# Kernel tuning notes

Hardware: AMD Instinct MI355X
Metric: run time of the kernel (lower is better)

The kernel has to match this reference:

```python
import jax, jax.numpy as jnp
import numpy as np

N, E, D, L = 50000, 600000, 128, 3
EPS = 1e-5


def _layer_norm(x, g, b):
    m = jnp.mean(x, axis=-1, keepdims=True)
    v = jnp.mean((x - m) ** 2, axis=-1, keepdims=True)
    return (x - m) * jax.lax.rsqrt(v + EPS) * g + b


def setup_inputs() -> dict:
    key = jax.random.key(0)
    ks = jax.random.split(key, 20)
    s = 1.0 / np.sqrt(D)
    inp = {
        "node": jax.random.normal(ks[0], (N, D), jnp.float32),
        "edge_attr": jax.random.uniform(ks[1], (E,), jnp.float32),
        # stacked per-layer parameters [L, ...]
        "W_rel": jax.random.uniform(ks[2], (L, D, D), jnp.float32, -s, s),
        "b_rel": jax.random.uniform(ks[3], (L, D), jnp.float32, -s, s),
        "W_root": jax.random.uniform(ks[4], (L, D, D), jnp.float32, -s, s),
        "ln1_g": jnp.ones((L, D), jnp.float32),
        "ln1_b": jnp.zeros((L, D), jnp.float32),
        "ln2_g": jnp.ones((L, D), jnp.float32),
        "ln2_b": jnp.zeros((L, D), jnp.float32),
        "W1": jax.random.uniform(ks[5], (L, D, D), jnp.float32, -s, s),
        "b1": jax.random.uniform(ks[6], (L, D), jnp.float32, -s, s),
        "W2": jax.random.uniform(ks[7], (L, D, D), jnp.float32, -s, s),
        "b2": jax.random.uniform(ks[8], (L, D), jnp.float32, -s, s),
        "jk_W": jax.random.uniform(ks[9], (L * D, D), jnp.float32, -1.0 / np.sqrt(L * D), 1.0 / np.sqrt(L * D)),
        "jk_b": jax.random.uniform(ks[10], (D,), jnp.float32, -1.0 / np.sqrt(L * D), 1.0 / np.sqrt(L * D)),
        "edge_index": jax.random.randint(ks[11], (2, E), 0, N, jnp.int64),
        "batch_ptr": jnp.sort(jax.random.randint(ks[12], (51,), 0, N, jnp.int64)),
    }
    return inp


def reference(node, edge_attr, W_rel, b_rel, W_root, ln1_g, ln1_b, ln2_g, ln2_b,
              W1, b1, W2, b2, jk_W, jk_b, edge_index, batch_ptr):
    src, dst = edge_index[0], edge_index[1]
    deg = jax.ops.segment_sum(jnp.ones((E,), node.dtype), dst, num_segments=N)
    inv_deg = 1.0 / jnp.maximum(deg, 1.0)  # nodes with no in-edges -> 0 aggregate
    outs = []
    for l in range(L):
        msg = node[src] * edge_attr[:, None]                       # [E, D] gather
        agg = jax.ops.segment_sum(msg, dst, num_segments=N)        # scatter-sum
        mean = agg * inv_deg[:, None]                              # mean aggregation
        # GraphConv: lin_rel(aggr) + lin_root(x); skip_connection=False
        node = mean @ W_rel[l] + b_rel[l] + node @ W_root[l]
        node = jax.nn.relu(_layer_norm(node @ W1[l] + b1[l], ln1_g[l], ln1_b[l]))
        node = jax.nn.relu(_layer_norm(node @ W2[l] + b2[l], ln2_g[l], ln2_b[l]))
        outs.append(node)
    jk = jnp.concatenate(outs, axis=-1)                            # [N, L*D]
    return jk @ jk_W + jk_b
```

## Files before the change

kernel.cpp:

```cpp
#include <hip/hip_runtime.h>

#define NN 50000
#define EE 600000
#define DD 128
#define CAP 64
#define BINS 196
#define NP (BINS * 256)
#define BINCAP 3584
#define BCSTRIDE 16
#define LDS_STRIDE 136
#define P1_EDGES 2048
#define P1_BLOCKS ((EE + P1_EDGES - 1) / P1_EDGES)

typedef __attribute__((ext_vector_type(8))) short bf16x8;
typedef __attribute__((ext_vector_type(4))) float f32x4;

__device__ __forceinline__ unsigned short f2bf(float f) {
    union { float f; unsigned u; } v; v.f = f;
    unsigned r = v.u + 0x7FFF + ((v.u >> 16) & 1);
    return (unsigned short)(r >> 16);
}
__device__ __forceinline__ float bflo(unsigned x) { return __uint_as_float(x << 16); }
__device__ __forceinline__ float bfhi(unsigned x) { return __uint_as_float(x & 0xffff0000u); }

__global__ __launch_bounds__(256) void fill_p1(
    const int* __restrict__ src, const int* __restrict__ dst, const float* __restrict__ ea,
    int* __restrict__ binCnt, unsigned long long* __restrict__ recs) {
    __shared__ int hist[BINS];
    __shared__ int lstart[BINS];
    __shared__ int gbase[BINS];
    __shared__ int scan[256];
    __shared__ unsigned long long srt[P1_EDGES];
    const int t = threadIdx.x;
    for (int i = t; i < BINS; i += 256) hist[i] = 0;
    __syncthreads();

    unsigned long long rec[8];
    int bin[8], rnk[8];
    bool val[8];
#pragma unroll
    for (int g = 0; g < 2; ++g) {
        int e0 = blockIdx.x * P1_EDGES + g * 1024 + t * 4;
        int4 dv, sv; float4 ev;
        if (e0 + 3 < EE) {
            dv = *(const int4*)&dst[e0];
            sv = *(const int4*)&src[e0];
            ev = *(const float4*)&ea[e0];
        } else {
            int* dp = (int*)&dv; int* sp = (int*)&sv; float* ep = (float*)&ev;
#pragma unroll
            for (int k = 0; k < 4; ++k) {
                int e = e0 + k;
                dp[k] = (e < EE) ? dst[e] : 0;
                sp[k] = (e < EE) ? src[e] : 0;
                ep[k] = (e < EE) ? ea[e] : 0.f;
            }
        }
#pragma unroll
        for (int k = 0; k < 4; ++k) {
            int i = g * 4 + k;
            int e = e0 + k;
            val[i] = (e < EE);
            int d = ((const int*)&dv)[k];
            unsigned w16 = (unsigned)__float2int_rn(((const float*)&ev)[k] * 65535.0f);
            if (w16 > 65535u) w16 = 65535u;
            rec[i] = ((unsigned long long)(unsigned)d << 32) |
                     (((unsigned)((const int*)&sv)[k]) << 16) | w16;
            bin[i] = d >> 8;
            rnk[i] = val[i] ? atomicAdd(&hist[bin[i]], 1) : 0;
        }
    }
    __syncthreads();
    scan[t] = (t < BINS) ? hist[t] : 0;
    __syncthreads();
#pragma unroll
    for (int off = 1; off < 256; off <<= 1) {
        int v = (t >= off) ? scan[t - off] : 0;
        __syncthreads();
        scan[t] += v;
        __syncthreads();
    }
    if (t < BINS) {
        lstart[t] = scan[t] - hist[t];
        gbase[t] = hist[t] ? atomicAdd(&binCnt[t * BCSTRIDE], hist[t]) : 0;
    }
    __syncthreads();
#pragma unroll
    for (int i = 0; i < 8; ++i)
        if (val[i]) srt[lstart[bin[i]] + rnk[i]] = rec[i];
    __syncthreads();
    const int total = scan[255];
    for (int j = t; j < total; j += 256) {
        unsigned long long r = srt[j];
        int b = (int)(r >> 40);
        int o = gbase[b] + (j - lstart[b]);
        if (o < BINCAP) recs[(size_t)b * BINCAP + o] = r;
    }
}

__global__ __launch_bounds__(256) void fill_p2(
    const int* __restrict__ binCnt, const unsigned long long* __restrict__ recs,
    int* __restrict__ cnt, unsigned* __restrict__ slots) {
    __shared__ int cl[128];
    __shared__ unsigned sl[128 * CAP];
    const int b = blockIdx.x >> 1, half = blockIdx.x & 1, t = threadIdx.x;
    if (t < 128) cl[t] = 0;
    __syncthreads();
    int n = binCnt[b * BCSTRIDE];
    if (n > BINCAP) n = BINCAP;
    const unsigned long long* rp = recs + (size_t)b * BINCAP;
    for (int j = t; j < n; j += 256) {
        unsigned long long r = rp[j];
        int dl = (int)(r >> 32) & 255;
        if ((dl >> 7) == half) {
            int p = atomicAdd(&cl[dl & 127], 1);
            if (p < CAP) sl[(dl & 127) * CAP + p] = (unsigned)r;
        }
    }
    __syncthreads();
    const int node0 = (b << 8) + (half << 7);
    if (t < 128) cnt[node0 + t] = cl[t];
    const uint4* s4 = (const uint4*)sl;
    uint4* g4 = (uint4*)(slots + (size_t)node0 * CAP);
    for (int i = t; i < 2048; i += 256) g4[i] = s4[i];
}

#define CONV_BLKS 6250
__global__ void prep_kernel(const float* __restrict__ nodef, unsigned short* __restrict__ node_bf,
                            const float* __restrict__ W_rel, const float* __restrict__ W_root,
                            const float* __restrict__ W1, const float* __restrict__ W2,
                            const float* __restrict__ jkW,
                            const float* __restrict__ b_rel, const float* __restrict__ b1,
                            float* __restrict__ bc, unsigned short* __restrict__ packed) {
    int b = blockIdx.x;
    if (b < 96) {
        int tg = b * 256 + threadIdx.x;
        int chunk = tg >> 11, r = tg & 2047;
        int lane = r & 63, tile = r >> 6;
        int kt = tile >> 3, nt = tile & 7;
        int quad = lane >> 4, n = lane & 15;
        int k0 = kt * 32 + quad * 8;
        int col = nt * 16 + n;
        union { unsigned short u[8]; uint4 v; } tmp;
        if (chunk < 6) {
            int l = (chunk < 3) ? chunk : chunk - 3;
            const float* A = ((chunk < 3) ? W_rel : W_root) + (size_t)l * 16384;
            const float* B = W1 + (size_t)l * 16384;
            float acc[8] = {0.f, 0.f, 0.f, 0.f, 0.f, 0.f, 0.f, 0.f};
            for (int k = 0; k < 128; ++k) {
                float bv = B[k * 128 + col];
#pragma unroll
                for (int j = 0; j < 8; ++j) acc[j] = fmaf(A[(k0 + j) * 128 + k], bv, acc[j]);
            }
#pragma unroll
            for (int j = 0; j < 8; ++j) tmp.u[j] = f2bf(acc[j]);
        } else {
            const float* s = (chunk < 9) ? (W2 + (size_t)(chunk - 6) * 16384)
                                         : (jkW + (size_t)(chunk - 9) * 16384);
#pragma unroll
            for (int j = 0; j < 8; ++j) tmp.u[j] = f2bf(s[(size_t)(k0 + j) * DD + col]);
        }
        *(uint4*)&packed[(size_t)tg * 8] = tmp.v;
    } else if (b == 96) {
        for (int o = threadIdx.x; o < 384; o += 256) {
            int l = o >> 7, j = o & 127;
            float s = 0.f;
            for (int k = 0; k < 128; ++k)
                s = fmaf(b_rel[l * 128 + k], W1[(size_t)l * 16384 + k * 128 + j], s);
            bc[o] = s + b1[o];
        }
    } else {
        int i = (b - 97) * 256 + threadIdx.x;
        float4 v = *(const float4*)&nodef[(size_t)i * 4];
        ushort4 o;
        o.x = f2bf(v.x); o.y = f2bf(v.y); o.z = f2bf(v.z); o.w = f2bf(v.w);
        *(ushort4*)&node_bf[(size_t)i * 4] = o;
    }
}

__global__ __launch_bounds__(256) void gather_mean_kernel(
    const unsigned short* __restrict__ feat,
    const unsigned* __restrict__ slots,
    const int* __restrict__ cnt,
    unsigned short* __restrict__ mean) {
    const int node = (int)((blockIdx.x * 256 + threadIdx.x) >> 6);
    if (node >= NN) return;
    const int lane = threadIdx.x & 63;
    const int g  = lane >> 4;
    const int h8 = (lane & 15) * 8;
    int c = cnt[node];
    if (c > CAP) c = CAP;
    const unsigned* sp = slots + (size_t)node * CAP;

    float acc[8] = {0.f, 0.f, 0.f, 0.f, 0.f, 0.f, 0.f, 0.f};
    const float wscale = 1.0f / 65535.0f;

    for (int j0 = 0; j0 < c; j0 += 16) {
        uint4 sv = *(const uint4*)&sp[j0 + g * 4];
        unsigned se[4] = {sv.x, sv.y, sv.z, sv.w};
#pragma unroll
        for (int t = 0; t < 4; ++t) {
            int idx = j0 + g * 4 + t;
            bool ok = idx < c;
            unsigned e = se[t];
            int   srcn = ok ? (int)(e >> 16) : 0;
            float w    = ok ? (float)(e & 0xffffu) * wscale : 0.0f;
            uint4 v = *(const uint4*)&feat[(size_t)srcn * DD + h8];
            acc[0] = fmaf(bflo(v.x), w, acc[0]);
            acc[1] = fmaf(bfhi(v.x), w, acc[1]);
            acc[2] = fmaf(bflo(v.y), w, acc[2]);
            acc[3] = fmaf(bfhi(v.y), w, acc[3]);
            acc[4] = fmaf(bflo(v.z), w, acc[4]);
            acc[5] = fmaf(bfhi(v.z), w, acc[5]);
            acc[6] = fmaf(bflo(v.w), w, acc[6]);
            acc[7] = fmaf(bfhi(v.w), w, acc[7]);
        }
    }

#pragma unroll
    for (int k = 0; k < 8; ++k) {
        acc[k] += __shfl_xor(acc[k], 16);
        acc[k] += __shfl_xor(acc[k], 32);
    }

    if (g == 0) {
        float id = 1.0f / fmaxf((float)c, 1.0f);
        union { unsigned short u[8]; uint4 v; } o;
#pragma unroll
        for (int k = 0; k < 8; ++k) o.u[k] = f2bf(acc[k] * id);
        *(uint4*)&mean[(size_t)node * DD + h8] = o.v;
    }
}

template <bool JK>
__global__ __launch_bounds__(256) void fused_layer(
    const unsigned short* __restrict__ mean, const unsigned short* __restrict__ nodef,
    const unsigned short* __restrict__ PWrel, const unsigned short* __restrict__ PWroot,
    const unsigned short* __restrict__ PW2,
    const float* __restrict__ bc, const float* __restrict__ ln1g, const float* __restrict__ ln1b,
    const float* __restrict__ b2, const float* __restrict__ ln2g, const float* __restrict__ ln2b,
    unsigned short* __restrict__ out,
    const unsigned short* __restrict__ o0, const unsigned short* __restrict__ o1,
    const unsigned short* __restrict__ PJ0, const unsigned short* __restrict__ PJ1,
    const unsigned short* __restrict__ PJ2,
    const float* __restrict__ jkb, float* __restrict__ fout) {
    __shared__ unsigned short relay[4][16 * LDS_STRIDE];
    const int lane = threadIdx.x & 63;
    const int wid  = threadIdx.x >> 6;
    const int mrow = blockIdx.x * 64 + wid * 16;
    if (mrow >= NN) return;

    const int quad = lane >> 4, n15 = lane & 15;
    const int kq   = quad * 8;
    unsigned short* wt = relay[wid];

    const unsigned short* Am = mean  + (size_t)(mrow + n15) * DD;
    const unsigned short* An = nodef + (size_t)(mrow + n15) * DD;

    f32x4 acc[8];
#pragma unroll
    for (int nt = 0; nt < 8; ++nt) acc[nt] = (f32x4){0.f, 0.f, 0.f, 0.f};
#pragma unroll
    for (int kt = 0; kt < 4; ++kt) {
        bf16x8 am = *(const bf16x8*)&Am[kt * 32 + kq];
        bf16x8 an = *(const bf16x8*)&An[kt * 32 + kq];
#pragma unroll
        for (int nt = 0; nt < 8; ++nt) {
            bf16x8 brel = *(const bf16x8*)&PWrel[(size_t)((kt * 8 + nt) * 64 + lane) * 8];
            acc[nt] = __builtin_amdgcn_mfma_f32_16x16x32_bf16(am, brel, acc[nt], 0, 0, 0);
            bf16x8 brt = *(const bf16x8*)&PWroot[(size_t)((kt * 8 + nt) * 64 + lane) * 8];
            acc[nt] = __builtin_amdgcn_mfma_f32_16x16x32_bf16(an, brt, acc[nt], 0, 0, 0);
        }
    }

    float x[8][4];
#pragma unroll
    for (int nt = 0; nt < 8; ++nt) {
        float bv = bc[nt * 16 + n15];
#pragma unroll
        for (int r = 0; r < 4; ++r) x[nt][r] = acc[nt][r] + bv;
    }
    {
        float s[4] = {0, 0, 0, 0}, q[4] = {0, 0, 0, 0};
#pragma unroll
        for (int nt = 0; nt < 8; ++nt)
#pragma unroll
            for (int r = 0; r < 4; ++r) { s[r] += x[nt][r]; q[r] += x[nt][r] * x[nt][r]; }
#pragma unroll
        for (int m = 1; m <= 8; m <<= 1)
#pragma unroll
            for (int r = 0; r < 4; ++r) { s[r] += __shfl_xor(s[r], m); q[r] += __shfl_xor(q[r], m); }
        const float inv = 1.0f / 128.0f;
#pragma unroll
        for (int r = 0; r < 4; ++r) {
            float mu = s[r] * inv;
            float rs = rsqrtf(fmaxf(q[r] * inv - mu * mu, 0.0f) + 1e-5f);
#pragma unroll
            for (int nt = 0; nt < 8; ++nt) {
                float g = ln1g[nt * 16 + n15], bb = ln1b[nt * 16 + n15];
                x[nt][r] = fmaxf((x[nt][r] - mu) * rs * g + bb, 0.0f);
            }
        }
    }

#pragma unroll
    for (int nt = 0; nt < 8; ++nt)
#pragma unroll
        for (int r = 0; r < 4; ++r)
            wt[(quad * 4 + r) * LDS_STRIDE + nt * 16 + n15] = f2bf(x[nt][r]);
    __asm__ __volatile__("s_waitcnt lgkmcnt(0)" ::: "memory");

    f32x4 acc2[8];
#pragma unroll
    for (int nt = 0; nt < 8; ++nt) acc2[nt] = (f32x4){0.f, 0.f, 0.f, 0.f};
#pragma unroll
    for (int kt = 0; kt < 4; ++kt) {
        bf16x8 ah = *(const bf16x8*)&wt[n15 * LDS_STRIDE + kt * 32 + kq];
#pragma unroll
        for (int nt = 0; nt < 8; ++nt) {
            bf16x8 bw = *(const bf16x8*)&PW2[(size_t)((kt * 8 + nt) * 64 + lane) * 8];
            acc2[nt] = __builtin_amdgcn_mfma_f32_16x16x32_bf16(ah, bw, acc2[nt], 0, 0, 0);
        }
    }
#pragma unroll
    for (int nt = 0; nt < 8; ++nt) {
        float bv = b2[nt * 16 + n15];
#pragma unroll
        for (int r = 0; r < 4; ++r) x[nt][r] = acc2[nt][r] + bv;
    }
    {
        float s[4] = {0, 0, 0, 0}, q[4] = {0, 0, 0, 0};
#pragma unroll
        for (int nt = 0; nt < 8; ++nt)
#pragma unroll
            for (int r = 0; r < 4; ++r) { s[r] += x[nt][r]; q[r] += x[nt][r] * x[nt][r]; }
#pragma unroll
        for (int m = 1; m <= 8; m <<= 1)
#pragma unroll
            for (int r = 0; r < 4; ++r) { s[r] += __shfl_xor(s[r], m); q[r] += __shfl_xor(q[r], m); }
        const float inv = 1.0f / 128.0f;
#pragma unroll
        for (int r = 0; r < 4; ++r) {
            float mu = s[r] * inv;
            float rs = rsqrtf(fmaxf(q[r] * inv - mu * mu, 0.0f) + 1e-5f);
#pragma unroll
            for (int nt = 0; nt < 8; ++nt) {
                float g = ln2g[nt * 16 + n15], bb = ln2b[nt * 16 + n15];
                x[nt][r] = fmaxf((x[nt][r] - mu) * rs * g + bb, 0.0f);
            }
        }
    }

    __asm__ __volatile__("s_waitcnt lgkmcnt(0)" ::: "memory");
#pragma unroll
    for (int nt = 0; nt < 8; ++nt)
#pragma unroll
        for (int r = 0; r < 4; ++r)
            wt[(quad * 4 + r) * LDS_STRIDE + nt * 16 + n15] = f2bf(x[nt][r]);
    __asm__ __volatile__("s_waitcnt lgkmcnt(0)" ::: "memory");

    if constexpr (!JK) {
#pragma unroll
        for (int i = 0; i < 4; ++i) {
            int s = i * 512 + lane * 8;
            int r = s >> 7, col = s & 127;
            uint4 v = *(const uint4*)&wt[r * LDS_STRIDE + col];
            *(uint4*)&out[(size_t)(mrow + r) * DD + col] = v;
        }
    } else {
        f32x4 accJ[8];
#pragma unroll
        for (int nt = 0; nt < 8; ++nt) accJ[nt] = (f32x4){0.f, 0.f, 0.f, 0.f};
#pragma unroll
        for (int kt = 0; kt < 4; ++kt) {
            bf16x8 ah = *(const bf16x8*)&wt[n15 * LDS_STRIDE + kt * 32 + kq];
#pragma unroll
            for (int nt = 0; nt < 8; ++nt) {
                bf16x8 bw = *(const bf16x8*)&PJ2[(size_t)((kt * 8 + nt) * 64 + lane) * 8];
                accJ[nt] = __builtin_amdgcn_mfma_f32_16x16x32_bf16(ah, bw, accJ[nt], 0, 0, 0);
            }
        }
        const unsigned short* A0 = o0 + (size_t)(mrow + n15) * DD;
        const unsigned short* A1 = o1 + (size_t)(mrow + n15) * DD;
#pragma unroll
        for (int kt = 0; kt < 4; ++kt) {
            bf16x8 a0 = *(const bf16x8*)&A0[kt * 32 + kq];
            bf16x8 a1 = *(const bf16x8*)&A1[kt * 32 + kq];
#pragma unroll
            for (int nt = 0; nt < 8; ++nt) {
                bf16x8 b0 = *(const bf16x8*)&PJ0[(size_t)((kt * 8 + nt) * 64 + lane) * 8];
                accJ[nt] = __builtin_amdgcn_mfma_f32_16x16x32_bf16(a0, b0, accJ[nt], 0, 0, 0);
                bf16x8 b1 = *(const bf16x8*)&PJ1[(size_t)((kt * 8 + nt) * 64 + lane) * 8];
                accJ[nt] = __builtin_amdgcn_mfma_f32_16x16x32_bf16(a1, b1, accJ[nt], 0, 0, 0);
            }
        }
#pragma unroll
        for (int nt = 0; nt < 8; ++nt) {
            float bv = jkb[nt * 16 + n15];
#pragma unroll
            for (int r = 0; r < 4; ++r)
                fout[(size_t)(mrow + quad * 4 + r) * DD + nt * 16 + n15] = accJ[nt][r] + bv;
        }
    }
}

extern "C" void kernel_launch(void* const* d_in, const int* in_sizes, int n_in,
                              void* d_out, int out_size, void* d_ws, size_t ws_size,
                              hipStream_t stream) {
    const float* node   = (const float*)d_in[0];
    const float* ea     = (const float*)d_in[1];
    const float* W_rel  = (const float*)d_in[2];
    const float* b_rel  = (const float*)d_in[3];
    const float* W_root = (const float*)d_in[4];
    const float* ln1_g  = (const float*)d_in[5];
    const float* ln1_b  = (const float*)d_in[6];
    const float* ln2_g  = (const float*)d_in[7];
    const float* ln2_b  = (const float*)d_in[8];
    const float* W1     = (const float*)d_in[9];
    const float* b1     = (const float*)d_in[10];
    const float* W2     = (const float*)d_in[11];
    const float* b2     = (const float*)d_in[12];
    const float* jk_W   = (const float*)d_in[13];
    const float* jk_b   = (const float*)d_in[14];
    const int*   ei     = (const int*)d_in[15];
    const int* srcI = ei;
    const int* dstI = ei + EE;

    char* ws = (char*)d_ws;
    size_t off = 0;
    auto alloc = [&](size_t bytes) {
        void* p = ws + off;
        off += (bytes + 255) & ~(size_t)255;
        return p;
    };
    int*                binCnt  = (int*)alloc((size_t)BINS * BCSTRIDE * 4);
    unsigned long long* recs    = (unsigned long long*)alloc((size_t)BINS * BINCAP * 8);
    int*                cnt     = (int*)alloc((size_t)NP * 4);
    unsigned*           slots   = (unsigned*)alloc((size_t)NP * CAP * 4);
    unsigned short*     node_bf = (unsigned short*)alloc((size_t)NN * DD * 2);
    unsigned short*     mean_bf = (unsigned short*)alloc((size_t)NN * DD * 2);
    unsigned short* outs_bf[2];
    for (int l = 0; l < 2; ++l) outs_bf[l] = (unsigned short*)alloc((size_t)NN * DD * 2);
    float*              bc      = (float*)alloc((size_t)3 * 128 * 4);
    unsigned short*     packed  = (unsigned short*)alloc((size_t)12 * 16384 * 2);

    hipMemsetAsync(binCnt, 0, (size_t)BINS * BCSTRIDE * 4, stream);
    fill_p1<<<P1_BLOCKS, 256, 0, stream>>>(srcI, dstI, ea, binCnt, recs);
    fill_p2<<<BINS * 2, 256, 0, stream>>>(binCnt, recs, cnt, slots);
    prep_kernel<<<97 + CONV_BLKS, 256, 0, stream>>>(
        node, node_bf, W_rel, W_root, W1, W2, jk_W, b_rel, b1, bc, packed);

    const int gblocks = (NN + 63) / 64;
    unsigned short* cur = node_bf;
    for (int l = 0; l < 3; ++l) {
        gather_mean_kernel<<<NN / 4, 256, 0, stream>>>(cur, slots, cnt, mean_bf);
        if (l < 2) {
            fused_layer<false><<<gblocks, 256, 0, stream>>>(
                mean_bf, cur,
                packed + (size_t)l * 16384, packed + (size_t)(3 + l) * 16384,
                packed + (size_t)(6 + l) * 16384,
                bc + (size_t)l * DD, ln1_g + (size_t)l * DD, ln1_b + (size_t)l * DD,
                b2 + (size_t)l * DD, ln2_g + (size_t)l * DD, ln2_b + (size_t)l * DD,
                outs_bf[l],
                nullptr, nullptr, nullptr, nullptr, nullptr, nullptr, nullptr);
            cur = outs_bf[l];
        } else {
            fused_layer<true><<<gblocks, 256, 0, stream>>>(
                mean_bf, cur,
                packed + (size_t)l * 16384, packed + (size_t)(3 + l) * 16384,
                packed + (size_t)(6 + l) * 16384,
                bc + (size_t)l * DD, ln1_g + (size_t)l * DD, ln1_b + (size_t)l * DD,
                b2 + (size_t)l * DD, ln2_g + (size_t)l * DD, ln2_b + (size_t)l * DD,
                nullptr,
                outs_bf[0], outs_bf[1],
                packed + (size_t)9 * 16384, packed + (size_t)10 * 16384, packed + (size_t)11 * 16384,
                jk_b, (float*)d_out);
        }
    }
}
```

Baseline: 290.5 us.

## Fuse neighbor mean gather into per-layer fused kernel via LDS staging

Removes the separate gather_mean kernel and its bf16 mean buffer round-trip. Each 64-thread block now handles 16 nodes: it gathers the weighted neighbor mean into LDS, then feeds it straight to the MFMA GEMMs with the root features. This saves a global write and read of the mean tensor plus one launch per layer. In exchange, each 16-lane group now walks one node's edges serially (4 per step instead of 16 in parallel), so gather parallelism and latency hiding per node drop. Single-wave blocks of 64 threads also change occupancy.

Measured after the change: 265.0 us. 1.1x faster.

```diff
diff --git a/kernel.cpp b/kernel.cpp
--- a/kernel.cpp
+++ b/kernel.cpp
@@ -178,63 +178,10 @@
     }
 }
 
-__global__ __launch_bounds__(256) void gather_mean_kernel(
+template <bool JK>
+__global__ __launch_bounds__(64, 4) void fused_layer(
     const unsigned short* __restrict__ feat,
-    const unsigned* __restrict__ slots,
-    const int* __restrict__ cnt,
-    unsigned short* __restrict__ mean) {
-    const int node = (int)((blockIdx.x * 256 + threadIdx.x) >> 6);
-    if (node >= NN) return;
-    const int lane = threadIdx.x & 63;
-    const int g  = lane >> 4;
-    const int h8 = (lane & 15) * 8;
-    int c = cnt[node];
-    if (c > CAP) c = CAP;
-    const unsigned* sp = slots + (size_t)node * CAP;
-
-    float acc[8] = {0.f, 0.f, 0.f, 0.f, 0.f, 0.f, 0.f, 0.f};
-    const float wscale = 1.0f / 65535.0f;
-
-    for (int j0 = 0; j0 < c; j0 += 16) {
-        uint4 sv = *(const uint4*)&sp[j0 + g * 4];
-        unsigned se[4] = {sv.x, sv.y, sv.z, sv.w};
-#pragma unroll
-        for (int t = 0; t < 4; ++t) {
-            int idx = j0 + g * 4 + t;
-            bool ok = idx < c;
-            unsigned e = se[t];
-            int   srcn = ok ? (int)(e >> 16) : 0;
-            float w    = ok ? (float)(e & 0xffffu) * wscale : 0.0f;
-            uint4 v = *(const uint4*)&feat[(size_t)srcn * DD + h8];
-            acc[0] = fmaf(bflo(v.x), w, acc[0]);
-            acc[1] = fmaf(bfhi(v.x), w, acc[1]);
-            acc[2] = fmaf(bflo(v.y), w, acc[2]);
-            acc[3] = fmaf(bfhi(v.y), w, acc[3]);
-            acc[4] = fmaf(bflo(v.z), w, acc[4]);
-            acc[5] = fmaf(bfhi(v.z), w, acc[5]);
-            acc[6] = fmaf(bflo(v.w), w, acc[6]);
-            acc[7] = fmaf(bfhi(v.w), w, acc[7]);
-        }
-    }
-
-#pragma unroll
-    for (int k = 0; k < 8; ++k) {
-        acc[k] += __shfl_xor(acc[k], 16);
-        acc[k] += __shfl_xor(acc[k], 32);
-    }
-
-    if (g == 0) {
-        float id = 1.0f / fmaxf((float)c, 1.0f);
-        union { unsigned short u[8]; uint4 v; } o;
-#pragma unroll
-        for (int k = 0; k < 8; ++k) o.u[k] = f2bf(acc[k] * id);
-        *(uint4*)&mean[(size_t)node * DD + h8] = o.v;
-    }
-}
-
-template <bool JK>
-__global__ __launch_bounds__(256) void fused_layer(
-    const unsigned short* __restrict__ mean, const unsigned short* __restrict__ nodef,
+    const unsigned* __restrict__ slots, const int* __restrict__ cnt,
     const unsigned short* __restrict__ PWrel, const unsigned short* __restrict__ PWroot,
     const unsigned short* __restrict__ PW2,
     const float* __restrict__ bc, const float* __restrict__ ln1g, const float* __restrict__ ln1b,
@@ -244,25 +191,60 @@
     const unsigned short* __restrict__ PJ0, const unsigned short* __restrict__ PJ1,
     const unsigned short* __restrict__ PJ2,
     const float* __restrict__ jkb, float* __restrict__ fout) {
-    __shared__ unsigned short relay[4][16 * LDS_STRIDE];
-    const int lane = threadIdx.x & 63;
-    const int wid  = threadIdx.x >> 6;
-    const int mrow = blockIdx.x * 64 + wid * 16;
-    if (mrow >= NN) return;
-
+    __shared__ __align__(16) unsigned short wt[16 * LDS_STRIDE];
+    const int lane = threadIdx.x;
+    const int mrow = blockIdx.x * 16;
     const int quad = lane >> 4, n15 = lane & 15;
     const int kq   = quad * 8;
-    unsigned short* wt = relay[wid];
-
-    const unsigned short* Am = mean  + (size_t)(mrow + n15) * DD;
-    const unsigned short* An = nodef + (size_t)(mrow + n15) * DD;
+
+    {
+        const int g4 = lane >> 4;
+        const int i8 = n15 * 8;
+        const float wscale = 1.0f / 65535.0f;
+#pragma unroll
+        for (int j4 = 0; j4 < 16; j4 += 4) {
+            const int node = mrow + j4 + g4;
+            int c = cnt[node];
+            if (c > CAP) c = CAP;
+            const unsigned* sp = slots + (size_t)node * CAP;
+            float acc[8] = {0.f, 0.f, 0.f, 0.f, 0.f, 0.f, 0.f, 0.f};
+            for (int j0 = 0; j0 < c; j0 += 4) {
+                uint4 sv = *(const uint4*)&sp[j0];
+                unsigned se[4] = {sv.x, sv.y, sv.z, sv.w};
+#pragma unroll
+                for (int t = 0; t < 4; ++t) {
+                    bool ok = (j0 + t) < c;
+                    unsigned e = se[t];
+                    int   srcn = ok ? (int)(e >> 16) : 0;
+                    float w    = ok ? (float)(e & 0xffffu) * wscale : 0.0f;
+                    uint4 v = *(const uint4*)&feat[(size_t)srcn * DD + i8];
+                    acc[0] = fmaf(bflo(v.x), w, acc[0]);
+                    acc[1] = fmaf(bfhi(v.x), w, acc[1]);
+                    acc[2] = fmaf(bflo(v.y), w, acc[2]);
+                    acc[3] = fmaf(bfhi(v.y), w, acc[3]);
+                    acc[4] = fmaf(bflo(v.z), w, acc[4]);
+                    acc[5] = fmaf(bfhi(v.z), w, acc[5]);
+                    acc[6] = fmaf(bflo(v.w), w, acc[6]);
+                    acc[7] = fmaf(bfhi(v.w), w, acc[7]);
+                }
+            }
+            float id = 1.0f / fmaxf((float)c, 1.0f);
+            union { unsigned short u[8]; uint4 v; } o;
+#pragma unroll
+            for (int k = 0; k < 8; ++k) o.u[k] = f2bf(acc[k] * id);
+            *(uint4*)&wt[(j4 + g4) * LDS_STRIDE + i8] = o.v;
+        }
+    }
+    __asm__ __volatile__("s_waitcnt lgkmcnt(0)" ::: "memory");
+
+    const unsigned short* An = feat + (size_t)(mrow + n15) * DD;
 
     f32x4 acc[8];
 #pragma unroll
     for (int nt = 0; nt < 8; ++nt) acc[nt] = (f32x4){0.f, 0.f, 0.f, 0.f};
 #pragma unroll
     for (int kt = 0; kt < 4; ++kt) {
-        bf16x8 am = *(const bf16x8*)&Am[kt * 32 + kq];
+        bf16x8 am = *(const bf16x8*)&wt[n15 * LDS_STRIDE + kt * 32 + kq];
         bf16x8 an = *(const bf16x8*)&An[kt * 32 + kq];
 #pragma unroll
         for (int nt = 0; nt < 8; ++nt) {
@@ -438,7 +420,6 @@
     int*                cnt     = (int*)alloc((size_t)NP * 4);
     unsigned*           slots   = (unsigned*)alloc((size_t)NP * CAP * 4);
     unsigned short*     node_bf = (unsigned short*)alloc((size_t)NN * DD * 2);
-    unsigned short*     mean_bf = (unsigned short*)alloc((size_t)NN * DD * 2);
     unsigned short* outs_bf[2];
     for (int l = 0; l < 2; ++l) outs_bf[l] = (unsigned short*)alloc((size_t)NN * DD * 2);
     float*              bc      = (float*)alloc((size_t)3 * 128 * 4);
@@ -450,13 +431,12 @@
     prep_kernel<<<97 + CONV_BLKS, 256, 0, stream>>>(
         node, node_bf, W_rel, W_root, W1, W2, jk_W, b_rel, b1, bc, packed);
 
-    const int gblocks = (NN + 63) / 64;
+    const int gblocks = NN / 16;
     unsigned short* cur = node_bf;
     for (int l = 0; l < 3; ++l) {
-        gather_mean_kernel<<<NN / 4, 256, 0, stream>>>(cur, slots, cnt, mean_bf);
         if (l < 2) {
-            fused_layer<false><<<gblocks, 256, 0, stream>>>(
-                mean_bf, cur,
+            fused_layer<false><<<gblocks, 64, 0, stream>>>(
+                cur, slots, cnt,
                 packed + (size_t)l * 16384, packed + (size_t)(3 + l) * 16384,
                 packed + (size_t)(6 + l) * 16384,
                 bc + (size_t)l * DD, ln1_g + (size_t)l * DD, ln1_b + (size_t)l * DD,
@@ -465,8 +445,8 @@
                 nullptr, nullptr, nullptr, nullptr, nullptr, nullptr, nullptr);
             cur = outs_bf[l];
         } else {
-            fused_layer<true><<<gblocks, 256, 0, stream>>>(
-                mean_bf, cur,
+            fused_layer<true><<<gblocks, 64, 0, stream>>>(
+                cur, slots, cnt,
                 packed + (size_t)l * 16384, packed + (size_t)(3 + l) * 16384,
                 packed + (size_t)(6 + l) * 16384,
                 bc + (size_t)l * DD, ln1_g + (size_t)l * DD, ln1_b + (size_t)l * DD,
```
